# Optimization experiments

Hardware: AMD Instinct MI355X
Metric: run time of the kernel (lower is better)

The kernel has to match this reference:

```python
import jax, jax.numpy as jnp
import numpy as np

EMB = 1024
HEADS = 16
HEAD_DIM = EMB // HEADS


def setup_inputs() -> dict:
    key = jax.random.key(0)
    ks = jax.random.split(key, 5)
    x = jax.random.normal(ks[0], (4, 2048, EMB), dtype=jnp.float32)
    # qkv Linear: weight [3*EMB, EMB] in torch; store transposed for x @ W
    Wqkv = jax.random.normal(ks[1], (EMB, 3 * EMB), dtype=jnp.float32) * (1.0 / np.sqrt(EMB))
    bqkv = jax.random.normal(ks[2], (3 * EMB,), dtype=jnp.float32) * 0.01
    Wout = jax.random.normal(ks[3], (EMB, EMB), dtype=jnp.float32) * (1.0 / np.sqrt(EMB))
    bout = jax.random.normal(ks[4], (EMB,), dtype=jnp.float32) * 0.01
    return {"x": x, "Wqkv": Wqkv, "bqkv": bqkv, "Wout": Wout, "bout": bout}


def reference(x, Wqkv, bqkv, Wout, bout):
    B, N, _ = x.shape
    qkv = x @ Wqkv + bqkv                              # [B, N, 3*EMB]
    qkv = qkv.reshape(B, N, 3, HEADS, HEAD_DIM)
    q, k, v = jnp.moveaxis(qkv, 2, 0)                  # each [B, N, H, D]
    q = jnp.swapaxes(q, 1, 2)                          # [B, H, N, D]
    k = jnp.swapaxes(k, 1, 2)
    v = jnp.swapaxes(v, 1, 2)
    scale = 1.0 / np.sqrt(HEAD_DIM).astype(np.float32)
    scores = jnp.einsum('bhqd,bhkd->bhqk', q, k) * scale
    attn = jax.nn.softmax(scores, axis=-1)             # dropout p=0 (eval)
    out = jnp.einsum('bhqk,bhkd->bhqd', attn, v)       # [B, H, N, D]
    out = jnp.swapaxes(out, 1, 2).reshape(B, N, EMB)
    return out @ Wout + bout
```

## Files before the change

### kernel.cpp

```cpp
#include <hip/hip_runtime.h>

#define SEQ   2048
#define EMBD  1024
#define HEADS 16
#define HDIM  64
#define MTOT  8192
#define LOG2E 1.44269504f

typedef __attribute__((ext_vector_type(8))) _Float16 half8;
typedef __attribute__((ext_vector_type(4))) _Float16 half4;
typedef __attribute__((ext_vector_type(2))) __fp16 fp16x2;
typedef __attribute__((ext_vector_type(4))) float f32x4;
typedef __attribute__((ext_vector_type(16))) float f32x16;

__device__ __forceinline__ f32x4 mfma16(half8 a, half8 b, f32x4 c) {
  return __builtin_amdgcn_mfma_f32_16x16x32_f16(a, b, c, 0, 0, 0);
}
__device__ __forceinline__ f32x16 mfma32(half8 a, half8 b, f32x16 c) {
  return __builtin_amdgcn_mfma_f32_32x32x16_f16(a, b, c, 0, 0, 0);
}

__device__ __forceinline__ void gload_lds16(const void* g, void* l) {
  __builtin_amdgcn_global_load_lds(
      (const __attribute__((address_space(1))) unsigned int*)g,
      (__attribute__((address_space(3))) unsigned int*)l, 16, 0, 0);
}

__device__ __forceinline__ unsigned pk2(float a, float b) {
  union { fp16x2 v; unsigned u; } t;
  t.v = __builtin_amdgcn_cvt_pkrtz(a, b);
  return t.u;
}

__global__ void k_cvt(const float* __restrict__ in, _Float16* __restrict__ out) {
  size_t i = (size_t)blockIdx.x * blockDim.x + threadIdx.x;
  const f32x4* in4 = (const f32x4*)in;
  f32x4 a = in4[2 * i], b = in4[2 * i + 1];
  half8 h;
  h[0] = (_Float16)a[0]; h[1] = (_Float16)a[1];
  h[2] = (_Float16)a[2]; h[3] = (_Float16)a[3];
  h[4] = (_Float16)b[0]; h[5] = (_Float16)b[1];
  h[6] = (_Float16)b[2]; h[7] = (_Float16)b[3];
  *(half8*)(out + i * 8) = h;
}

__global__ __launch_bounds__(256) void k_transpose(const float* __restrict__ in,
                                                   _Float16* __restrict__ out,
                                                   int R, int C) {
  __shared__ _Float16 tile[64][65];
  const int tid = threadIdx.x;
  const int r0 = blockIdx.y * 64, c0 = blockIdx.x * 64;
  const int tr = tid >> 6;
  const int tc = tid & 63;
  #pragma unroll
  for (int i = 0; i < 16; ++i) {
    const int r = i * 4 + tr;
    tile[r][tc] = (_Float16)in[(size_t)(r0 + r) * C + c0 + tc];
  }
  __syncthreads();
  #pragma unroll
  for (int i = 0; i < 16; ++i) {
    const int cc = i * 4 + tr;
    out[(size_t)(c0 + cc) * R + r0 + tc] = tile[tc][cc];
  }
}

template<int EPI>
__global__ __launch_bounds__(256) void k_gemm(
    const _Float16* __restrict__ A, const _Float16* __restrict__ Bt,
    const float* __restrict__ bias, float* __restrict__ outf,
    _Float16* __restrict__ q, _Float16* __restrict__ k, _Float16* __restrict__ vt)
{
  __shared__ _Float16 sm[2 * 128 * 64];
  _Float16* sA = sm;
  _Float16* sB = sm + 128 * 64;
  const int tid = threadIdx.x;
  const int l = tid & 63, g = l >> 4, c = l & 15;
  const int w = tid >> 6;
  const int wm = (w >> 1) * 64, wn = (w & 1) * 64;
  const int rowBase = blockIdx.y * 128;
  const int colBase = blockIdx.x * 128;

  f32x4 acc[4][4] = {};

  const _Float16* Ag = A + (size_t)(rowBase + (tid >> 3)) * 1024 + (tid & 7) * 8;
  const _Float16* Bg = Bt + (size_t)(colBase + (tid >> 3)) * 1024 + (tid & 7) * 8;
  _Float16* la = sA + tid * 8;
  _Float16* lb = sB + tid * 8;

  for (int kt = 0; kt < 16; ++kt) {
    const _Float16* ag = Ag + kt * 64;
    const _Float16* bg = Bg + kt * 64;
    #pragma unroll
    for (int i = 0; i < 4; ++i) {
      gload_lds16(ag + (size_t)i * 32 * 1024, la + i * 256 * 8);
      gload_lds16(bg + (size_t)i * 32 * 1024, lb + i * 256 * 8);
    }
    __syncthreads();
    #pragma unroll
    for (int kk = 0; kk < 2; ++kk) {
      half8 af[4], bf[4];
      #pragma unroll
      for (int t = 0; t < 4; ++t)
        af[t] = *(const half8*)(sA + (wm + t * 16 + c) * 64 + kk * 32 + g * 8);
      #pragma unroll
      for (int t = 0; t < 4; ++t)
        bf[t] = *(const half8*)(sB + (wn + t * 16 + c) * 64 + kk * 32 + g * 8);
      #pragma unroll
      for (int mt = 0; mt < 4; ++mt)
        #pragma unroll
        for (int nt = 0; nt < 4; ++nt)
          acc[mt][nt] = mfma16(af[mt], bf[nt], acc[mt][nt]);
    }
    __syncthreads();
  }

  #pragma unroll
  for (int mt = 0; mt < 4; ++mt) {
    #pragma unroll
    for (int nt = 0; nt < 4; ++nt) {
      const int col = colBase + wn + nt * 16 + c;
      const float bv = bias[col];
      #pragma unroll
      for (int r = 0; r < 4; ++r) {
        const int row = rowBase + wm + mt * 16 + g * 4 + r;
        const float val = acc[mt][nt][r] + bv;
        if constexpr (EPI == 0) {
          const int s = col >> 10, h = (col >> 6) & 15, d = col & 63;
          const int b = row >> 11, n = row & 2047;
          const int bh = b * HEADS + h;
          const _Float16 hv = (_Float16)val;
          if (s == 2)      vt[((size_t)bh * HDIM + d) * SEQ + n] = hv;
          else if (s == 1) k [((size_t)bh * SEQ + n) * HDIM + d] = hv;
          else             q [((size_t)bh * SEQ + n) * HDIM + d] = hv;
        } else {
          outf[(size_t)row * EMBD + col] = val;
        }
      }
    }
  }
}

__global__ __launch_bounds__(512, 4) void k_attn(
    const _Float16* __restrict__ q, const _Float16* __restrict__ kg,
    const _Float16* __restrict__ vt, _Float16* __restrict__ aout)
{
  __shared__ _Float16 sm[64 * 72 * 2 + 8 * 32 * 76];
  _Float16* Ks = sm;
  _Float16* Vs = sm + 64 * 72;
  const int tid = threadIdx.x;
  const int w = tid >> 6, l = tid & 63;
  const int q32 = l & 31, hi = l >> 5;
  _Float16* Pw = sm + 2 * 64 * 72 + w * 32 * 76;

  const int orig = blockIdx.x;
  const int lb = (orig & 7) * 64 + (orig >> 3);
  const int bh = lb >> 3;
  const int n0 = (lb & 7) * 256 + w * 32;

  const _Float16* qb = q  + (size_t)bh * SEQ * HDIM;
  const _Float16* kb = kg + (size_t)bh * SEQ * HDIM;
  const _Float16* vb = vt + (size_t)bh * HDIM * SEQ;
  const int row0 = tid >> 3, cb = tid & 7;

  half8 aq[4];
  #pragma unroll
  for (int ch = 0; ch < 4; ++ch) {
    half8 t = *(const half8*)(qb + (size_t)(n0 + q32) * HDIM + ch * 16 + hi * 8);
    aq[ch] = t * (_Float16)0.125f;
  }

  float m_ = -1e30f, l_ = 0.f;
  f32x16 o0 = {}, o1 = {};

  half8 kr = *(const half8*)(kb + (size_t)tid * 8);
  half8 vr = *(const half8*)(vb + (size_t)row0 * SEQ + cb * 8);

  for (int kt = 0; kt < SEQ / 64; ++kt) {
    __syncthreads();
    *(half8*)(Ks + row0 * 72 + cb * 8) = kr;
    *(half8*)(Vs + row0 * 72 + cb * 8) = vr;
    if (kt + 1 < SEQ / 64) {
      kr = *(const half8*)(kb + (size_t)(kt + 1) * 64 * HDIM + (size_t)tid * 8);
      vr = *(const half8*)(vb + (size_t)row0 * SEQ + (kt + 1) * 64 + cb * 8);
    }
    __syncthreads();

    f32x16 s0 = {}, s1 = {};
    __builtin_amdgcn_s_setprio(1);
    #pragma unroll
    for (int ch = 0; ch < 4; ++ch) {
      half8 ak0 = *(const half8*)(Ks + q32 * 72 + ch * 16 + hi * 8);
      half8 ak1 = *(const half8*)(Ks + (32 + q32) * 72 + ch * 16 + hi * 8);
      s0 = mfma32(ak0, aq[ch], s0);
      s1 = mfma32(ak1, aq[ch], s1);
    }
    __builtin_amdgcn_s_setprio(0);

    float mx = fmaxf(s0[0], s1[0]);
    #pragma unroll
    for (int e = 1; e < 16; ++e) mx = fmaxf(mx, fmaxf(s0[e], s1[e]));

    if (__any(mx > m_ + 8.0f)) {
      const float fm = fmaxf(mx, __shfl_xor(mx, 32, 64));
      const float mo = m_;
      const float mn = fmaxf(mo, fm);
      const float cor = __builtin_amdgcn_exp2f((mo - mn) * LOG2E);
      m_ = mn;
      l_ *= cor;
      #pragma unroll
      for (int e = 0; e < 16; ++e) { o0[e] *= cor; o1[e] *= cor; }
    }

    float rs = 0.f;
    #pragma unroll
    for (int e = 0; e < 16; ++e) {
      s0[e] = __builtin_amdgcn_exp2f((s0[e] - m_) * LOG2E);
      s1[e] = __builtin_amdgcn_exp2f((s1[e] - m_) * LOG2E);
      rs += s0[e] + s1[e];
    }
    l_ += rs;

    _Float16* prow = Pw + q32 * 76;
    #pragma unroll
    for (int j = 0; j < 4; ++j) {
      union { unsigned u[2]; half4 h; } t0, t1;
      t0.u[0] = pk2(s0[4 * j], s0[4 * j + 1]);
      t0.u[1] = pk2(s0[4 * j + 2], s0[4 * j + 3]);
      t1.u[0] = pk2(s1[4 * j], s1[4 * j + 1]);
      t1.u[1] = pk2(s1[4 * j + 2], s1[4 * j + 3]);
      *(half4*)(prow + 8 * j + 4 * hi) = t0.h;
      *(half4*)(prow + 32 + 8 * j + 4 * hi) = t1.h;
    }

    __builtin_amdgcn_s_setprio(1);
    #pragma unroll
    for (int ch = 0; ch < 4; ++ch) {
      half8 pf  = *(const half8*)(Pw + q32 * 76 + ch * 16 + hi * 8);
      half8 av0 = *(const half8*)(Vs + q32 * 72 + ch * 16 + hi * 8);
      half8 av1 = *(const half8*)(Vs + (32 + q32) * 72 + ch * 16 + hi * 8);
      o0 = mfma32(av0, pf, o0);
      o1 = mfma32(av1, pf, o1);
    }
    __builtin_amdgcn_s_setprio(0);
  }

  float lt = l_ + __shfl_xor(l_, 32, 64);
  const float rl = __builtin_amdgcn_rcpf(lt);

  _Float16* Ot = Pw;
  #pragma unroll
  for (int dh = 0; dh < 2; ++dh) {
    #pragma unroll
    for (int j = 0; j < 4; ++j) {
      union { unsigned u[2]; half4 h; } t;
      if (dh == 0) {
        t.u[0] = pk2(o0[4 * j] * rl, o0[4 * j + 1] * rl);
        t.u[1] = pk2(o0[4 * j + 2] * rl, o0[4 * j + 3] * rl);
      } else {
        t.u[0] = pk2(o1[4 * j] * rl, o1[4 * j + 1] * rl);
        t.u[1] = pk2(o1[4 * j + 2] * rl, o1[4 * j + 3] * rl);
      }
      *(half4*)(Ot + q32 * 76 + dh * 32 + 8 * j + 4 * hi) = t.h;
    }
  }

  const int b = bh >> 4, h = bh & 15;
  #pragma unroll
  for (int i = 0; i < 4; ++i) {
    const int qq = 8 * i + (l >> 3);
    half8 v = *(const half8*)(Ot + qq * 76 + (l & 7) * 8);
    *(half8*)(aout + (size_t)(b * SEQ + n0 + qq) * EMBD + h * HDIM + (l & 7) * 8) = v;
  }
}

extern "C" void kernel_launch(void* const* d_in, const int* in_sizes, int n_in,
                              void* d_out, int out_size, void* d_ws, size_t ws_size,
                              hipStream_t stream) {
  const float* x    = (const float*)d_in[0];
  const float* Wqkv = (const float*)d_in[1];
  const float* bqkv = (const float*)d_in[2];
  const float* Wout = (const float*)d_in[3];
  const float* bout = (const float*)d_in[4];
  float* out = (float*)d_out;

  _Float16* ws    = (_Float16*)d_ws;
  _Float16* xh    = ws;
  _Float16* wqkvt = xh + (size_t)MTOT * EMBD;
  _Float16* woutt = wqkvt + (size_t)3 * EMBD * EMBD;
  _Float16* qbuf  = woutt + (size_t)EMBD * EMBD;
  _Float16* kbuf  = qbuf + (size_t)MTOT * EMBD;
  _Float16* vtbuf = kbuf + (size_t)MTOT * EMBD;
  _Float16* aout  = xh;

  k_cvt<<<4096, 256, 0, stream>>>(x, xh);
  k_transpose<<<dim3(48, 16), 256, 0, stream>>>(Wqkv, wqkvt, 1024, 3072);
  k_transpose<<<dim3(16, 16), 256, 0, stream>>>(Wout, woutt, 1024, 1024);
  k_gemm<0><<<dim3(24, 64), 256, 0, stream>>>(xh, wqkvt, bqkv, nullptr,
                                              qbuf, kbuf, vtbuf);
  k_attn<<<512, 512, 0, stream>>>(qbuf, kbuf, vtbuf, aout);
  k_gemm<1><<<dim3(8, 64), 256, 0, stream>>>(aout, woutt, bout, out,
                                             nullptr, nullptr, nullptr);
}
```

Measured before the change: 247.6 us.

## Fold log2e into Q scale, compute row sums via MFMA, double K/V tile

Multiplies log2(e) into the Q pre-scale so the softmax exponent needs only a subtraction, and computes the row-sum denominator with an extra MFMA against a ones vector instead of VALU adds and a cross-lane shuffle. The max reduction becomes a tree, and K/V tiles grow to 128 keys per sync, halving barrier and global-load rounds. In exchange it adds MFMA work per chunk, uses more LDS that may cut occupancy, and sums the denominator from fp16-rounded probabilities.

```diff
diff --git a/kernel.cpp b/kernel.cpp
--- a/kernel.cpp
+++ b/kernel.cpp
@@ -5,7 +5,6 @@
 #define HEADS 16
 #define HDIM  64
 #define MTOT  8192
-#define LOG2E 1.44269504f
 
 typedef __attribute__((ext_vector_type(8))) _Float16 half8;
 typedef __attribute__((ext_vector_type(4))) _Float16 half4;
@@ -145,13 +144,13 @@
     const _Float16* __restrict__ q, const _Float16* __restrict__ kg,
     const _Float16* __restrict__ vt, _Float16* __restrict__ aout)
 {
-  __shared__ _Float16 sm[64 * 72 * 2 + 8 * 32 * 76];
+  __shared__ _Float16 sm[128 * 72 + 64 * 136 + 8 * 32 * 76];
   _Float16* Ks = sm;
-  _Float16* Vs = sm + 64 * 72;
+  _Float16* Vs = sm + 128 * 72;
   const int tid = threadIdx.x;
   const int w = tid >> 6, l = tid & 63;
   const int q32 = l & 31, hi = l >> 5;
-  _Float16* Pw = sm + 2 * 64 * 72 + w * 32 * 76;
+  _Float16* Pw = sm + 128 * 72 + 64 * 136 + w * 32 * 76;
 
   const int orig = blockIdx.x;
   const int lb = (orig & 7) * 64 + (orig >> 3);
@@ -163,90 +162,116 @@
   const _Float16* vb = vt + (size_t)bh * HDIM * SEQ;
   const int row0 = tid >> 3, cb = tid & 7;
 
+  const _Float16 qs = (_Float16)(0.125f * 1.44269504f);
   half8 aq[4];
   #pragma unroll
   for (int ch = 0; ch < 4; ++ch) {
     half8 t = *(const half8*)(qb + (size_t)(n0 + q32) * HDIM + ch * 16 + hi * 8);
-    aq[ch] = t * (_Float16)0.125f;
-  }
-
-  float m_ = -1e30f, l_ = 0.f;
-  f32x16 o0 = {}, o1 = {};
-
-  half8 kr = *(const half8*)(kb + (size_t)tid * 8);
-  half8 vr = *(const half8*)(vb + (size_t)row0 * SEQ + cb * 8);
-
-  for (int kt = 0; kt < SEQ / 64; ++kt) {
+    aq[ch] = t * qs;
+  }
+
+  half8 ones;
+  #pragma unroll
+  for (int i = 0; i < 8; ++i) ones[i] = (_Float16)1.0f;
+
+  float m_ = -1e30f;
+  f32x16 o0 = {}, o1 = {}, lacc = {};
+
+  half8 kr0 = *(const half8*)(kb + (size_t)tid * 8);
+  half8 kr1 = *(const half8*)(kb + 4096 + (size_t)tid * 8);
+  half8 vr0 = *(const half8*)(vb + (size_t)row0 * SEQ + cb * 8);
+  half8 vr1 = *(const half8*)(vb + (size_t)row0 * SEQ + 64 + cb * 8);
+
+  for (int kt = 0; kt < SEQ / 128; ++kt) {
     __syncthreads();
-    *(half8*)(Ks + row0 * 72 + cb * 8) = kr;
-    *(half8*)(Vs + row0 * 72 + cb * 8) = vr;
-    if (kt + 1 < SEQ / 64) {
-      kr = *(const half8*)(kb + (size_t)(kt + 1) * 64 * HDIM + (size_t)tid * 8);
-      vr = *(const half8*)(vb + (size_t)row0 * SEQ + (kt + 1) * 64 + cb * 8);
+    *(half8*)(Ks + row0 * 72 + cb * 8) = kr0;
+    *(half8*)(Ks + (row0 + 64) * 72 + cb * 8) = kr1;
+    *(half8*)(Vs + row0 * 136 + cb * 8) = vr0;
+    *(half8*)(Vs + row0 * 136 + 64 + cb * 8) = vr1;
+    if (kt + 1 < SEQ / 128) {
+      const _Float16* kn = kb + (size_t)(kt + 1) * 128 * HDIM;
+      kr0 = *(const half8*)(kn + (size_t)tid * 8);
+      kr1 = *(const half8*)(kn + 4096 + (size_t)tid * 8);
+      const _Float16* vn = vb + (size_t)row0 * SEQ + (kt + 1) * 128;
+      vr0 = *(const half8*)(vn + cb * 8);
+      vr1 = *(const half8*)(vn + 64 + cb * 8);
     }
     __syncthreads();
 
-    f32x16 s0 = {}, s1 = {};
-    __builtin_amdgcn_s_setprio(1);
-    #pragma unroll
-    for (int ch = 0; ch < 4; ++ch) {
-      half8 ak0 = *(const half8*)(Ks + q32 * 72 + ch * 16 + hi * 8);
-      half8 ak1 = *(const half8*)(Ks + (32 + q32) * 72 + ch * 16 + hi * 8);
-      s0 = mfma32(ak0, aq[ch], s0);
-      s1 = mfma32(ak1, aq[ch], s1);
-    }
-    __builtin_amdgcn_s_setprio(0);
-
-    float mx = fmaxf(s0[0], s1[0]);
-    #pragma unroll
-    for (int e = 1; e < 16; ++e) mx = fmaxf(mx, fmaxf(s0[e], s1[e]));
-
-    if (__any(mx > m_ + 8.0f)) {
-      const float fm = fmaxf(mx, __shfl_xor(mx, 32, 64));
-      const float mo = m_;
-      const float mn = fmaxf(mo, fm);
-      const float cor = __builtin_amdgcn_exp2f((mo - mn) * LOG2E);
-      m_ = mn;
-      l_ *= cor;
-      #pragma unroll
-      for (int e = 0; e < 16; ++e) { o0[e] *= cor; o1[e] *= cor; }
-    }
-
-    float rs = 0.f;
-    #pragma unroll
-    for (int e = 0; e < 16; ++e) {
-      s0[e] = __builtin_amdgcn_exp2f((s0[e] - m_) * LOG2E);
-      s1[e] = __builtin_amdgcn_exp2f((s1[e] - m_) * LOG2E);
-      rs += s0[e] + s1[e];
-    }
-    l_ += rs;
-
-    _Float16* prow = Pw + q32 * 76;
-    #pragma unroll
-    for (int j = 0; j < 4; ++j) {
-      union { unsigned u[2]; half4 h; } t0, t1;
-      t0.u[0] = pk2(s0[4 * j], s0[4 * j + 1]);
-      t0.u[1] = pk2(s0[4 * j + 2], s0[4 * j + 3]);
-      t1.u[0] = pk2(s1[4 * j], s1[4 * j + 1]);
-      t1.u[1] = pk2(s1[4 * j + 2], s1[4 * j + 3]);
-      *(half4*)(prow + 8 * j + 4 * hi) = t0.h;
-      *(half4*)(prow + 32 + 8 * j + 4 * hi) = t1.h;
-    }
-
-    __builtin_amdgcn_s_setprio(1);
-    #pragma unroll
-    for (int ch = 0; ch < 4; ++ch) {
-      half8 pf  = *(const half8*)(Pw + q32 * 76 + ch * 16 + hi * 8);
-      half8 av0 = *(const half8*)(Vs + q32 * 72 + ch * 16 + hi * 8);
-      half8 av1 = *(const half8*)(Vs + (32 + q32) * 72 + ch * 16 + hi * 8);
-      o0 = mfma32(av0, pf, o0);
-      o1 = mfma32(av1, pf, o1);
-    }
-    __builtin_amdgcn_s_setprio(0);
-  }
-
-  float lt = l_ + __shfl_xor(l_, 32, 64);
-  const float rl = __builtin_amdgcn_rcpf(lt);
+    #pragma unroll
+    for (int p = 0; p < 2; ++p) {
+      const _Float16* Kp = Ks + p * 64 * 72;
+      const _Float16* Vp = Vs + p * 64;
+
+      f32x16 s0 = {}, s1 = {};
+      __builtin_amdgcn_s_setprio(1);
+      #pragma unroll
+      for (int ch = 0; ch < 4; ++ch) {
+        half8 ak0 = *(const half8*)(Kp + q32 * 72 + ch * 16 + hi * 8);
+        half8 ak1 = *(const half8*)(Kp + (32 + q32) * 72 + ch * 16 + hi * 8);
+        s0 = mfma32(ak0, aq[ch], s0);
+        s1 = mfma32(ak1, aq[ch], s1);
+      }
+      __builtin_amdgcn_s_setprio(0);
+
+      float u0 = fmaxf(s0[0], s1[0]),   u1 = fmaxf(s0[1], s1[1]);
+      float u2 = fmaxf(s0[2], s1[2]),   u3 = fmaxf(s0[3], s1[3]);
+      float u4 = fmaxf(s0[4], s1[4]),   u5 = fmaxf(s0[5], s1[5]);
+      float u6 = fmaxf(s0[6], s1[6]),   u7 = fmaxf(s0[7], s1[7]);
+      float u8 = fmaxf(s0[8], s1[8]),   u9 = fmaxf(s0[9], s1[9]);
+      float ua = fmaxf(s0[10], s1[10]), ub = fmaxf(s0[11], s1[11]);
+      float uc = fmaxf(s0[12], s1[12]), ud = fmaxf(s0[13], s1[13]);
+      float ue = fmaxf(s0[14], s1[14]), uf = fmaxf(s0[15], s1[15]);
+      u0 = fmaxf(u0, u8); u1 = fmaxf(u1, u9); u2 = fmaxf(u2, ua);
+      u3 = fmaxf(u3, ub); u4 = fmaxf(u4, uc); u5 = fmaxf(u5, ud);
+      u6 = fmaxf(u6, ue); u7 = fmaxf(u7, uf);
+      u0 = fmaxf(u0, u4); u1 = fmaxf(u1, u5); u2 = fmaxf(u2, u6); u3 = fmaxf(u3, u7);
+      const float mx = fmaxf(fmaxf(u0, u1), fmaxf(u2, u3));
+
+      if (__any(mx > m_ + 11.5416f)) {
+        const float fm = fmaxf(mx, __shfl_xor(mx, 32, 64));
+        const float mo = m_;
+        const float mn = fmaxf(mo, fm);
+        const float cor = __builtin_amdgcn_exp2f(mo - mn);
+        m_ = mn;
+        lacc[0] *= cor;
+        #pragma unroll
+        for (int e = 0; e < 16; ++e) { o0[e] *= cor; o1[e] *= cor; }
+      }
+
+      #pragma unroll
+      for (int e = 0; e < 16; ++e) {
+        s0[e] = __builtin_amdgcn_exp2f(s0[e] - m_);
+        s1[e] = __builtin_amdgcn_exp2f(s1[e] - m_);
+      }
+
+      _Float16* prow = Pw + q32 * 76;
+      #pragma unroll
+      for (int j = 0; j < 4; ++j) {
+        union { unsigned u[2]; half4 h; } t0, t1;
+        t0.u[0] = pk2(s0[4 * j], s0[4 * j + 1]);
+        t0.u[1] = pk2(s0[4 * j + 2], s0[4 * j + 3]);
+        t1.u[0] = pk2(s1[4 * j], s1[4 * j + 1]);
+        t1.u[1] = pk2(s1[4 * j + 2], s1[4 * j + 3]);
+        *(half4*)(prow + 8 * j + 4 * hi) = t0.h;
+        *(half4*)(prow + 32 + 8 * j + 4 * hi) = t1.h;
+      }
+
+      __builtin_amdgcn_s_setprio(1);
+      #pragma unroll
+      for (int ch = 0; ch < 4; ++ch) {
+        half8 pf  = *(const half8*)(Pw + q32 * 76 + ch * 16 + hi * 8);
+        half8 av0 = *(const half8*)(Vp + q32 * 136 + ch * 16 + hi * 8);
+        half8 av1 = *(const half8*)(Vp + (32 + q32) * 136 + ch * 16 + hi * 8);
+        o0 = mfma32(av0, pf, o0);
+        o1 = mfma32(av1, pf, o1);
+        lacc = mfma32(ones, pf, lacc);
+      }
+      __builtin_amdgcn_s_setprio(0);
+    }
+  }
+
+  const float rl = __builtin_amdgcn_rcpf(lacc[0]);
 
   _Float16* Ot = Pw;
   #pragma unroll
```

Result: slower. 255.2 us (+3.1%).
